# Optimization experiments

Measured on AMD Instinct MI355X. Metric: run time of the kernel, lower is better.

Reference implementation:

```python
import jax, jax.numpy as jnp
import numpy as np

# Static configuration (mirrors init_kwargs / forward defaults)
KERNEL = 128          # WW
INDEX_BACK = 32768    # number of highest-frequency bins discarded
PADDING = 0           # padding_count (padding=None in forward)

def next_power2(x):
    return int(2 ** np.ceil(np.log2(x)))

def setup_inputs() -> dict:
    key = jax.random.key(0)
    k1, k2, k3 = jax.random.split(key, 3)
    N, C, W = 32, 8, 65536
    F = 16
    x = jax.random.normal(k1, (N, C, W), dtype=jnp.float32)
    weight = jax.random.normal(k2, (F, C, KERNEL), dtype=jnp.float32) * 0.1
    bias = jax.random.normal(k3, (F,), dtype=jnp.float32)
    return {"x": x, "weight": weight, "bias": bias}

def reference(x, weight, bias):
    # x: [N, C, W], weight: [F, C, WW], bias: [F]
    N, C, W = x.shape
    F, _, WW = weight.shape
    pad = PADDING
    out_W = W - WW + 1 + 2 * pad
    # fft size sized to also hold the backward dout correlation, then next pow2
    init_fft_size_input = W + 2 * pad + 2 * (WW - 1)
    init_fft_size_dout = out_W + 2 * (WW - 1)
    init_fft_size = next_power2(max(init_fft_size_input, init_fft_size_dout))
    half = init_fft_size // 2 + 1

    # rfft with implicit zero-padding to init_fft_size (input left-padded by `pad`)
    x_p = jnp.pad(x, ((0, 0), (0, 0), (pad, 0)))
    xfft = jnp.fft.rfft(x_p, n=init_fft_size, axis=-1)      # [N, C, half]
    yfft = jnp.fft.rfft(weight, n=init_fft_size, axis=-1)   # [F, C, half]

    # spectral compression: drop the INDEX_BACK highest-frequency bins
    keep = half - INDEX_BACK
    xfft = xfft[..., :keep]
    yfft = yfft[..., :keep]

    # cross-correlation in frequency domain (torch conv == correlation),
    # summing over input channels C in the spectrum (linearity of irfft)
    outfft = jnp.einsum('nck,fck->nfk', xfft, jnp.conj(yfft))  # [N, F, keep]

    # zero-pad discarded high frequencies back and invert
    outfft = jnp.pad(outfft, ((0, 0), (0, 0), (0, half - keep)))
    out = jnp.fft.irfft(outfft, n=init_fft_size, axis=-1)[..., :out_W]  # [N, F, out_W]

    out = out + bias[None, :, None]
    return out
```

## Files before the change

kernel.cpp:

```cpp
#include <hip/hip_runtime.h>

namespace {

constexpr int NFFT  = 65536;
constexpr int KEEPK = 32768;
constexpr int OUTW  = 65409;
constexpr size_t YBYTES = (size_t)128 * 32769 * 8;

typedef float2 cplx;

__device__ __forceinline__ cplx cmk(float x, float y){ return make_float2(x, y); }
__device__ __forceinline__ cplx cadd(cplx a, cplx b){ return cmk(a.x+b.x, a.y+b.y); }
__device__ __forceinline__ cplx csub(cplx a, cplx b){ return cmk(a.x-b.x, a.y-b.y); }
__device__ __forceinline__ cplx cmul(cplx a, cplx b){ return cmk(a.x*b.x - a.y*b.y, a.x*b.y + a.y*b.x); }
__device__ __forceinline__ cplx cmulj(cplx a, cplx b){
  return cmk(a.x*b.x + a.y*b.y, a.y*b.x - a.x*b.y); }

template<int DIR>
__device__ __forceinline__ void dft16(cplx v[16]) {
  const float C1 = 0.92387953251128674f;
  const float S1 = 0.38268343236508977f;
  const float C2 = 0.70710678118654752f;
  const float WR[16]  = {1.f, C1, C2, S1, 0.f, -S1, -C2, -C1, -1.f, -C1, -C2, -S1, 0.f, S1, C2, C1};
  const float WIF[16] = {0.f, -S1, -C2, -C1, -1.f, -C1, -C2, -S1, 0.f, S1, C2, C1, 1.f, C1, C2, S1};
  cplx s[16];
  #pragma unroll
  for (int n2 = 0; n2 < 4; ++n2) {
    cplx a = v[n2], b = v[n2+4], c = v[n2+8], d = v[n2+12];
    cplx ac = cadd(a,c), am = csub(a,c), bd = cadd(b,d), bm = csub(b,d);
    cplx x0 = cadd(ac, bd), x2 = csub(ac, bd), x1, x3;
    if (DIR == -1) { x1 = cmk(am.x + bm.y, am.y - bm.x); x3 = cmk(am.x - bm.y, am.y + bm.x); }
    else           { x1 = cmk(am.x - bm.y, am.y + bm.x); x3 = cmk(am.x + bm.y, am.y - bm.x); }
    s[0*4+n2] = x0;
    {
      int e1 = (n2*1) & 15, e2 = (n2*2) & 15, e3 = (n2*3) & 15;
      cplx w1 = cmk(WR[e1], (DIR==-1)? WIF[e1] : -WIF[e1]);
      cplx w2 = cmk(WR[e2], (DIR==-1)? WIF[e2] : -WIF[e2]);
      cplx w3 = cmk(WR[e3], (DIR==-1)? WIF[e3] : -WIF[e3]);
      s[1*4+n2] = cmul(x1, w1);
      s[2*4+n2] = cmul(x2, w2);
      s[3*4+n2] = cmul(x3, w3);
    }
  }
  #pragma unroll
  for (int t1 = 0; t1 < 4; ++t1) {
    cplx a = s[t1*4+0], b = s[t1*4+1], c = s[t1*4+2], d = s[t1*4+3];
    cplx ac = cadd(a,c), am = csub(a,c), bd = cadd(b,d), bm = csub(b,d);
    cplx x0 = cadd(ac,bd), x2 = csub(ac,bd), x1, x3;
    if (DIR == -1) { x1 = cmk(am.x + bm.y, am.y - bm.x); x3 = cmk(am.x - bm.y, am.y + bm.x); }
    else           { x1 = cmk(am.x - bm.y, am.y + bm.x); x3 = cmk(am.x + bm.y, am.y - bm.x); }
    v[t1+0] = x0; v[t1+4] = x1; v[t1+8] = x2; v[t1+12] = x3;
  }
}

template<int DIR>
__global__ __launch_bounds__(256)
void fft_pass_a(const cplx* __restrict__ in, long inStride, int inLen,
                cplx* __restrict__ T) {
  int blk = blockIdx.x;
  int seq = blk >> 4;
  int B0  = (blk & 15) << 4;
  int t = threadIdx.x;
  __shared__ cplx tile[16][260];
  {
    const cplx* src = in + (long)seq * inStride;
    int cb = t & 15, rg = t >> 4;
    #pragma unroll
    for (int i = 0; i < 16; ++i) {
      int a = i*16 + rg;
      int sIdx = a*256 + B0 + cb;
      cplx v = (sIdx < inLen) ? src[sIdx] : cmk(0.f, 0.f);
      tile[cb][a] = v;
    }
  }
  __syncthreads();
  int cc = t >> 4, j = t & 15;
  cplx x[16];
  #pragma unroll
  for (int a1 = 0; a1 < 16; ++a1) x[a1] = tile[cc][a1*16 + j];
  dft16<DIR>(x);
  {
    float sn, cs;
    __sincosf((float)DIR * 6.28318530717958648f * (float)j * (1.0f/256.0f), &sn, &cs);
    cplx r = cmk(cs, sn), cur = r;
    #pragma unroll
    for (int t1 = 1; t1 < 16; ++t1) { x[t1] = cmul(x[t1], cur); cur = cmul(cur, r); }
  }
  __syncthreads();
  #pragma unroll
  for (int t1 = 0; t1 < 16; ++t1) tile[cc][t1*16 + ((j + t1) & 15)] = x[t1];
  __syncthreads();
  #pragma unroll
  for (int a2 = 0; a2 < 16; ++a2) x[a2] = tile[cc][j*16 + ((a2 + j) & 15)];
  dft16<DIR>(x);
  int b = B0 + cc;
  cplx* dst = T + (long)seq * NFFT + (long)b * 256;
  {
    float sn, cs;
    __sincosf((float)DIR * 6.28318530717958648f * (float)(b*j) * (1.0f/65536.0f), &sn, &cs);
    cplx cur = cmk(cs, sn);
    __sincosf((float)DIR * 6.28318530717958648f * (float)b * (1.0f/4096.0f), &sn, &cs);
    cplx stp = cmk(cs, sn);
    #pragma unroll
    for (int t2 = 0; t2 < 16; ++t2) {
      dst[j + 16*t2] = cmul(x[t2], cur);
      cur = cmul(cur, stp);
    }
  }
}

template<int DIR, int MODE>
__global__ __launch_bounds__(256)
void fft_pass_b(const cplx* __restrict__ T, cplx* __restrict__ outZ,
                float* __restrict__ outR, const float* __restrict__ bias,
                int seqBase) {
  int blk = blockIdx.x;
  int seq = blk >> 4;
  int K0  = (blk & 15) << 4;
  int t = threadIdx.x;
  __shared__ cplx tile[16][260];
  {
    const cplx* src = T + (long)seq * NFFT;
    int ck = t & 15, rg = t >> 4;
    #pragma unroll
    for (int i = 0; i < 16; ++i) {
      int b = i*16 + rg;
      tile[ck][b] = src[b*256 + K0 + ck];
    }
  }
  __syncthreads();
  int cc = t >> 4, j = t & 15;
  cplx x[16];
  #pragma unroll
  for (int a1 = 0; a1 < 16; ++a1) x[a1] = tile[cc][a1*16 + j];
  dft16<DIR>(x);
  {
    float sn, cs;
    __sincosf((float)DIR * 6.28318530717958648f * (float)j * (1.0f/256.0f), &sn, &cs);
    cplx r = cmk(cs, sn), cur = r;
    #pragma unroll
    for (int t1 = 1; t1 < 16; ++t1) { x[t1] = cmul(x[t1], cur); cur = cmul(cur, r); }
  }
  __syncthreads();
  #pragma unroll
  for (int t1 = 0; t1 < 16; ++t1) tile[cc][t1*16 + ((j + t1) & 15)] = x[t1];
  __syncthreads();
  #pragma unroll
  for (int a2 = 0; a2 < 16; ++a2) x[a2] = tile[cc][j*16 + ((a2 + j) & 15)];
  dft16<DIR>(x);
  __syncthreads();
  #pragma unroll
  for (int t2 = 0; t2 < 16; ++t2) tile[cc][j + 16*t2] = x[t2];
  __syncthreads();
  int ck2 = t & 15, rg2 = t >> 4;
  if (MODE == 0) {
    cplx* dst = outZ + (long)seq * NFFT + K0 + ck2;
    #pragma unroll
    for (int i = 0; i < 16; ++i) {
      int k2 = i*16 + rg2;
      dst[256*k2] = tile[ck2][k2];
    }
  } else {
    const float sc = 1.0f / 65536.0f;
    int gseq = seqBase + seq;
    float bf = bias[gseq & 15];
    float* dst = outR + (long)gseq * OUTW;
    #pragma unroll
    for (int i = 0; i < 16; ++i) {
      int k2 = i*16 + rg2;
      int s  = K0 + ck2 + 256*k2;
      int tp = 2*s;
      cplx v = tile[ck2][k2];
      if (tp < OUTW)     dst[tp]   = v.x * sc + bf;
      if (tp + 1 < OUTW) dst[tp+1] = v.y * sc + bf;
    }
  }
}

__global__ __launch_bounds__(256)
void weight_spec(const float* __restrict__ wgt, cplx* __restrict__ Y) {
  int seq = blockIdx.y;
  int k = blockIdx.x * 256 + threadIdx.x;
  __shared__ float wt[128];
  if (threadIdx.x < 128) wt[threadIdx.x] = wgt[seq * 128 + threadIdx.x];
  __syncthreads();
  if (k > KEEPK) return;
  float sn, cs;
  __sincosf(-3.14159265358979324f * (float)k * (1.0f/65536.0f), &sn, &cs);
  cplx r  = cmk(cs, sn);
  cplx r2 = cmul(r, r);
  cplx r4 = cmul(r2, r2);
  cplx r8 = cmul(r4, r4);
  cplx av[8];
  #pragma unroll
  for (int v = 0; v < 8; ++v) av[v] = cmk(0.f, 0.f);
  cplx C = cmk(1.f, 0.f);
  #pragma unroll
  for (int u = 0; u < 16; ++u) {
    #pragma unroll
    for (int v = 0; v < 8; ++v) {
      float w = wt[u*8 + v];
      av[v].x += w * C.x;
      av[v].y += w * C.y;
    }
    C = cmul(C, r8);
  }
  cplx acc = av[7];
  #pragma unroll
  for (int v = 6; v >= 0; --v) acc = cadd(av[v], cmul(r, acc));
  Y[(long)seq * 32769 + k] = acc;
}

__global__ __launch_bounds__(256)
void mac_pack(const cplx* __restrict__ Zx, const cplx* __restrict__ Yspec,
              cplx* __restrict__ Zout, int Bn) {
  int K0 = blockIdx.x * 32;
  int tid = threadIdx.x;
  int kk = tid & 31;
  int ng = tid >> 5;
  int k = K0 + kk;
  __shared__ cplx Yt[16][8][32];
  for (int e = tid; e < 16*8*32; e += 256) {
    int f = e >> 8;
    int c = (e >> 5) & 7;
    int q = e & 31;
    int kg = K0 + q;
    Yt[f][c][q] = (kg <= KEEPK) ? Yspec[(long)(f*8 + c) * 32769 + kg] : cmk(0.f, 0.f);
  }
  __syncthreads();
  if (k > KEEPK) return;
  float sn, cs;
  __sincosf(-3.14159265358979324f * (float)k * (1.0f/65536.0f), &sn, &cs);
  cplx w  = cmk(cs, sn);
  cplx wp = cmk(cs, -sn);
  int nPerG = (Bn + 7) >> 3;
  for (int nn = 0; nn < nPerG; ++nn) {
    int ln = ng * nPerG + nn;
    if (ln >= Bn) break;
    cplx X[8];
    #pragma unroll
    for (int c = 0; c < 8; ++c) {
      const cplx* Z = Zx + (long)(ln*8 + c) * NFFT;
      cplx zk = Z[k];
      cplx zm = Z[(NFFT - k) & (NFFT - 1)];
      cplx E = cmk(0.5f*(zk.x + zm.x), 0.5f*(zk.y - zm.y));
      cplx D = cmk(zk.x - zm.x, zk.y + zm.y);
      cplx O = cmk(0.5f*D.y, -0.5f*D.x);
      X[c] = cadd(E, cmul(w, O));
    }
    #pragma unroll
    for (int f = 0; f < 16; ++f) {
      cplx S = cmk(0.f, 0.f);
      #pragma unroll
      for (int c = 0; c < 8; ++c) S = cadd(S, cmulj(X[c], Yt[f][c][kk]));
      cplx* Zo = Zout + (long)(ln*16 + f) * NFFT;
      if (k == KEEPK) {
        Zo[k] = cmk(S.x, -S.y);
      } else {
        cplx E2 = cmk(0.5f*S.x, 0.5f*S.y);
        cplx O2 = cmul(wp, E2);
        Zo[k] = cmk(E2.x - O2.y, E2.y + O2.x);
        if (k > 0)
          Zo[NFFT - k] = cmk(E2.x + O2.y, O2.x - E2.y);
      }
    }
  }
}

}

extern "C" void kernel_launch(void* const* d_in, const int* in_sizes, int n_in,
                              void* d_out, int out_size, void* d_ws, size_t ws_size,
                              hipStream_t stream) {
  const cplx*  x    = (const cplx*)d_in[0];
  const float* wgt  = (const float*)d_in[1];
  const float* bias = (const float*)d_in[2];
  float* out = (float*)d_out;

  static const int BnOpt[5] = {16, 8, 4, 2, 1};
  int ti = 4;
  for (int i = 0; i < 5; ++i) {
    size_t zxb = (size_t)BnOpt[i] * 8  * NFFT * sizeof(cplx);
    size_t zob = (size_t)BnOpt[i] * 16 * NFFT * sizeof(cplx);
    if (YBYTES + zxb + 2 * zob <= ws_size) { ti = i; break; }
  }
  const int Bn = BnOpt[ti];
  const size_t zxb = (size_t)Bn * 8  * NFFT * sizeof(cplx);
  const size_t zob = (size_t)Bn * 16 * NFFT * sizeof(cplx);

  char* ws = (char*)d_ws;
  cplx* Y  = (cplx*)ws;
  cplx* Zx = (cplx*)(ws + YBYTES);
  cplx* Zo = (cplx*)(ws + YBYTES + zxb);
  cplx* T  = (cplx*)(ws + YBYTES + zxb + zob);

  weight_spec<<<dim3(129, 128), dim3(256), 0, stream>>>(wgt, Y);

  for (int n0 = 0; n0 < 32; n0 += Bn) {
    int sx = Bn * 8;
    int so = Bn * 16;
    fft_pass_a<-1><<<dim3(sx*16), dim3(256), 0, stream>>>(x + (long)n0*8*32768, 32768, 32768, T);
    fft_pass_b<-1,0><<<dim3(sx*16), dim3(256), 0, stream>>>(T, Zx, (float*)nullptr, (const float*)nullptr, 0);
    mac_pack<<<dim3(1025), dim3(256), 0, stream>>>(Zx, Y, Zo, Bn);
    fft_pass_a<1><<<dim3(so*16), dim3(256), 0, stream>>>(Zo, 65536, 65536, T);
    fft_pass_b<1,1><<<dim3(so*16), dim3(256), 0, stream>>>(T, (cplx*)nullptr, out, bias, n0*16);
  }
}
```

Measured before the change: 662.9 us.

## Swizzle FFT shared tiles, shorten twiddle chains, raise occupancy hints

Replaces the padded 16x260 shared tile with an unpadded 4096-entry tile that uses an XOR swizzle, which shrinks LDS per block while still avoiding bank conflicts. Twiddle factors are now built from binary powers (r, r^2, r^4, r^8) instead of a serial multiply chain, which shortens dependency chains at the cost of a few extra multiplies. It also adds a min-blocks hint of 5 to the launch bounds of the FFT and MAC kernels to push up occupancy, which risks register spills.

```diff
diff --git a/kernel.cpp b/kernel.cpp
--- a/kernel.cpp
+++ b/kernel.cpp
@@ -15,6 +15,8 @@
 __device__ __forceinline__ cplx cmul(cplx a, cplx b){ return cmk(a.x*b.x - a.y*b.y, a.x*b.y + a.y*b.x); }
 __device__ __forceinline__ cplx cmulj(cplx a, cplx b){
   return cmk(a.x*b.x + a.y*b.y, a.y*b.x - a.x*b.y); }
+
+#define TIX(row, a) (((row) << 8) + (((a) ^ ((row) * 17)) & 255))
 
 template<int DIR>
 __device__ __forceinline__ void dft16(cplx v[16]) {
@@ -54,14 +56,33 @@
 }
 
 template<int DIR>
-__global__ __launch_bounds__(256)
+__device__ __forceinline__ void stage_twiddle(cplx x[16], float ang) {
+  float sn, cs;
+  __sincosf(ang, &sn, &cs);
+  cplx r1 = cmk(cs, sn);
+  cplx r2 = cmul(r1, r1);
+  cplx r4 = cmul(r2, r2);
+  cplx r8 = cmul(r4, r4);
+  #pragma unroll
+  for (int t1 = 1; t1 < 16; ++t1) {
+    cplx m = x[t1];
+    if (t1 & 1) m = cmul(m, r1);
+    if (t1 & 2) m = cmul(m, r2);
+    if (t1 & 4) m = cmul(m, r4);
+    if (t1 & 8) m = cmul(m, r8);
+    x[t1] = m;
+  }
+}
+
+template<int DIR>
+__global__ __launch_bounds__(256, 5)
 void fft_pass_a(const cplx* __restrict__ in, long inStride, int inLen,
                 cplx* __restrict__ T) {
   int blk = blockIdx.x;
   int seq = blk >> 4;
   int B0  = (blk & 15) << 4;
   int t = threadIdx.x;
-  __shared__ cplx tile[16][260];
+  __shared__ cplx tile[4096];
   {
     const cplx* src = in + (long)seq * inStride;
     int cb = t & 15, rg = t >> 4;
@@ -70,47 +91,48 @@
       int a = i*16 + rg;
       int sIdx = a*256 + B0 + cb;
       cplx v = (sIdx < inLen) ? src[sIdx] : cmk(0.f, 0.f);
-      tile[cb][a] = v;
+      tile[TIX(cb, a)] = v;
     }
   }
   __syncthreads();
   int cc = t >> 4, j = t & 15;
   cplx x[16];
   #pragma unroll
-  for (int a1 = 0; a1 < 16; ++a1) x[a1] = tile[cc][a1*16 + j];
+  for (int a1 = 0; a1 < 16; ++a1) x[a1] = tile[TIX(cc, a1*16 + j)];
   dft16<DIR>(x);
-  {
-    float sn, cs;
-    __sincosf((float)DIR * 6.28318530717958648f * (float)j * (1.0f/256.0f), &sn, &cs);
-    cplx r = cmk(cs, sn), cur = r;
-    #pragma unroll
-    for (int t1 = 1; t1 < 16; ++t1) { x[t1] = cmul(x[t1], cur); cur = cmul(cur, r); }
-  }
-  __syncthreads();
-  #pragma unroll
-  for (int t1 = 0; t1 < 16; ++t1) tile[cc][t1*16 + ((j + t1) & 15)] = x[t1];
-  __syncthreads();
-  #pragma unroll
-  for (int a2 = 0; a2 < 16; ++a2) x[a2] = tile[cc][j*16 + ((a2 + j) & 15)];
+  stage_twiddle<DIR>(x, (float)DIR * 6.28318530717958648f * (float)j * (1.0f/256.0f));
+  __syncthreads();
+  #pragma unroll
+  for (int t1 = 0; t1 < 16; ++t1) tile[TIX(cc, t1*16 + ((j + t1) & 15))] = x[t1];
+  __syncthreads();
+  #pragma unroll
+  for (int a2 = 0; a2 < 16; ++a2) x[a2] = tile[TIX(cc, j*16 + ((a2 + j) & 15))];
   dft16<DIR>(x);
   int b = B0 + cc;
   cplx* dst = T + (long)seq * NFFT + (long)b * 256;
   {
     float sn, cs;
     __sincosf((float)DIR * 6.28318530717958648f * (float)(b*j) * (1.0f/65536.0f), &sn, &cs);
-    cplx cur = cmk(cs, sn);
+    cplx base = cmk(cs, sn);
     __sincosf((float)DIR * 6.28318530717958648f * (float)b * (1.0f/4096.0f), &sn, &cs);
-    cplx stp = cmk(cs, sn);
+    cplx s1 = cmk(cs, sn);
+    cplx s2 = cmul(s1, s1);
+    cplx s4 = cmul(s2, s2);
+    cplx s8 = cmul(s4, s4);
     #pragma unroll
     for (int t2 = 0; t2 < 16; ++t2) {
-      dst[j + 16*t2] = cmul(x[t2], cur);
-      cur = cmul(cur, stp);
+      cplx m = cmul(x[t2], base);
+      if (t2 & 1) m = cmul(m, s1);
+      if (t2 & 2) m = cmul(m, s2);
+      if (t2 & 4) m = cmul(m, s4);
+      if (t2 & 8) m = cmul(m, s8);
+      dst[j + 16*t2] = m;
     }
   }
 }
 
 template<int DIR, int MODE>
-__global__ __launch_bounds__(256)
+__global__ __launch_bounds__(256, 5)
 void fft_pass_b(const cplx* __restrict__ T, cplx* __restrict__ outZ,
                 float* __restrict__ outR, const float* __restrict__ bias,
                 int seqBase) {
@@ -118,39 +140,33 @@
   int seq = blk >> 4;
   int K0  = (blk & 15) << 4;
   int t = threadIdx.x;
-  __shared__ cplx tile[16][260];
+  __shared__ cplx tile[4096];
   {
     const cplx* src = T + (long)seq * NFFT;
     int ck = t & 15, rg = t >> 4;
     #pragma unroll
     for (int i = 0; i < 16; ++i) {
       int b = i*16 + rg;
-      tile[ck][b] = src[b*256 + K0 + ck];
+      tile[TIX(ck, b)] = src[b*256 + K0 + ck];
     }
   }
   __syncthreads();
   int cc = t >> 4, j = t & 15;
   cplx x[16];
   #pragma unroll
-  for (int a1 = 0; a1 < 16; ++a1) x[a1] = tile[cc][a1*16 + j];
+  for (int a1 = 0; a1 < 16; ++a1) x[a1] = tile[TIX(cc, a1*16 + j)];
   dft16<DIR>(x);
-  {
-    float sn, cs;
-    __sincosf((float)DIR * 6.28318530717958648f * (float)j * (1.0f/256.0f), &sn, &cs);
-    cplx r = cmk(cs, sn), cur = r;
-    #pragma unroll
-    for (int t1 = 1; t1 < 16; ++t1) { x[t1] = cmul(x[t1], cur); cur = cmul(cur, r); }
-  }
-  __syncthreads();
-  #pragma unroll
-  for (int t1 = 0; t1 < 16; ++t1) tile[cc][t1*16 + ((j + t1) & 15)] = x[t1];
-  __syncthreads();
-  #pragma unroll
-  for (int a2 = 0; a2 < 16; ++a2) x[a2] = tile[cc][j*16 + ((a2 + j) & 15)];
+  stage_twiddle<DIR>(x, (float)DIR * 6.28318530717958648f * (float)j * (1.0f/256.0f));
+  __syncthreads();
+  #pragma unroll
+  for (int t1 = 0; t1 < 16; ++t1) tile[TIX(cc, t1*16 + ((j + t1) & 15))] = x[t1];
+  __syncthreads();
+  #pragma unroll
+  for (int a2 = 0; a2 < 16; ++a2) x[a2] = tile[TIX(cc, j*16 + ((a2 + j) & 15))];
   dft16<DIR>(x);
   __syncthreads();
   #pragma unroll
-  for (int t2 = 0; t2 < 16; ++t2) tile[cc][j + 16*t2] = x[t2];
+  for (int t2 = 0; t2 < 16; ++t2) tile[TIX(cc, j + 16*t2)] = x[t2];
   __syncthreads();
   int ck2 = t & 15, rg2 = t >> 4;
   if (MODE == 0) {
@@ -158,7 +174,7 @@
     #pragma unroll
     for (int i = 0; i < 16; ++i) {
       int k2 = i*16 + rg2;
-      dst[256*k2] = tile[ck2][k2];
+      dst[256*k2] = tile[TIX(ck2, k2)];
     }
   } else {
     const float sc = 1.0f / 65536.0f;
@@ -170,7 +186,7 @@
       int k2 = i*16 + rg2;
       int s  = K0 + ck2 + 256*k2;
       int tp = 2*s;
-      cplx v = tile[ck2][k2];
+      cplx v = tile[TIX(ck2, k2)];
       if (tp < OUTW)     dst[tp]   = v.x * sc + bf;
       if (tp + 1 < OUTW) dst[tp+1] = v.y * sc + bf;
     }
@@ -211,7 +227,7 @@
   Y[(long)seq * 32769 + k] = acc;
 }
 
-__global__ __launch_bounds__(256)
+__global__ __launch_bounds__(256, 5)
 void mac_pack(const cplx* __restrict__ Zx, const cplx* __restrict__ Yspec,
               cplx* __restrict__ Zout, int Bn) {
   int K0 = blockIdx.x * 32;
```

Measured after the change: 745.8 us. 1.13x slower.
